# Kernel tuning notes

Measured on AMD Instinct MI355X. Metric: run time of the kernel, lower is better.

## Reference

```python
import jax, jax.numpy as jnp
import numpy as np

B_SZ, SEQ, ENC = 8, 768, 21
PRED = 192
N_HIPPO = 256
MULTISCALE = [1, 2, 4]
MODES = 32  # min(32, min(pred_len, seq_len)//2)


def _transition(N):
    Q = np.arange(N, dtype=np.float64)
    R = (2 * Q + 1)[:, None]
    j, i = np.meshgrid(Q, Q)
    A = np.where(i < j, -1.0, (-1.0) ** (i - j + 1)) * R
    Bv = (-1.0) ** Q[:, None] * R
    return A, Bv


def _hippo_discrete(N, dt):
    # scipy cont2discrete bilinear (Tustin, alpha=0.5)
    A, Bv = _transition(N)
    I = np.eye(N)
    M = I - (dt / 2.0) * A
    Ad = np.linalg.solve(M, I + (dt / 2.0) * A)
    Bd = np.linalg.solve(M, dt * Bv).squeeze(-1)
    return (jnp.asarray(Ad, jnp.float32), jnp.asarray(Bd, jnp.float32))


def _eval_matrix(N, dt):
    # ss.eval_legendre(arange(N)[:,None], 1-2*vals).T  -> (len(vals), N)
    vals = np.arange(0.0, 1.0, dt)
    x = 1.0 - 2.0 * vals
    P = np.zeros((len(vals), N), dtype=np.float64)
    P[:, 0] = 1.0
    if N > 1:
        P[:, 1] = x
    for n in range(1, N - 1):
        P[:, n + 1] = ((2 * n + 1) * x * P[:, n] - n * P[:, n - 1]) / (n + 1)
    return jnp.asarray(P, jnp.float32)


def _legt(x, A, Bv):
    # x: (B, E, L) -> HiPPO coeffs (B, E, N, L) via linear recurrence
    fs = jnp.moveaxis(x, -1, 0)  # (L, B, E)
    c0 = jnp.zeros(x.shape[:-1] + (A.shape[0],), x.dtype)

    def step(c, f):
        c = c @ A.T + f[..., None] * Bv
        return c, c

    _, cs = jax.lax.scan(step, c0, fs)  # (L, B, E, N)
    return jnp.moveaxis(cs, 0, -1)  # (B, E, N, L)


def _spectral(x, wr, wi):
    # x: (B, E, N_in, L); wr/wi: (N_in, N_out, MODES)
    L = x.shape[-1]
    xft = jnp.fft.rfft(x)
    a = xft[..., :MODES]
    o_re = jnp.einsum('bjix,iox->bjox', a.real, wr) - jnp.einsum('bjix,iox->bjox', a.imag, wi)
    o_im = jnp.einsum('bjix,iox->bjox', a.real, wi) + jnp.einsum('bjix,iox->bjox', a.imag, wr)
    o = jax.lax.complex(o_re, o_im)
    pad = jnp.zeros(o.shape[:-1] + (L // 2 + 1 - MODES,), o.dtype)
    return jnp.fft.irfft(jnp.concatenate([o, pad], axis=-1), n=L)


def _forward(x_enc, affine_weight, affine_bias, spec_wr, spec_wi, mlp_w, mlp_b):
    means = jax.lax.stop_gradient(jnp.mean(x_enc, axis=1, keepdims=True))
    xc = x_enc - means
    stdev = jax.lax.stop_gradient(jnp.sqrt(jnp.var(xc, axis=1, keepdims=True) + 1e-5))
    xc = xc / stdev
    xc = xc * affine_weight + affine_bias

    x_decs = []
    for i, m in enumerate(MULTISCALE):
        dt = 1.0 / PRED / m
        A, Bv = _hippo_discrete(N_HIPPO, dt)
        ev = _eval_matrix(N_HIPPO, dt)  # (m*PRED, N)
        x_in = xc[:, -m * PRED:]  # (B, L, E)
        c = _legt(jnp.transpose(x_in, (0, 2, 1)), A, Bv)  # (B, E, N, L)
        out1 = _spectral(c, spec_wr[i], spec_wi[i])  # (B, E, N, L)
        # seq_len >= pred_len branch: take time index PRED-1 along L
        x_dec_c = out1[:, :, :, PRED - 1].swapaxes(-1, -1)  # (B, E, N) after transpose(2,3) + index
        x_dec_c = out1.swapaxes(2, 3)[:, :, PRED - 1, :]  # (B, E, N)
        x_dec = x_dec_c @ ev[-PRED:, :].T  # (B, E, PRED)
        x_decs.append(x_dec)

    xd = jnp.stack(x_decs, axis=-1)  # (B, E, PRED, 3)
    xd = jnp.einsum('beps,os->bepo', xd, mlp_w) + mlp_b  # Linear(3,1)
    xd = jnp.transpose(xd[..., 0], (0, 2, 1))  # (B, PRED, E)
    xd = (xd - affine_bias) / (affine_weight + 1e-10)
    xd = xd * stdev + means
    return xd


def setup_inputs() -> dict:
    key = jax.random.key(0)
    ks = jax.random.split(key, 8)
    scale = 1.0 / (N_HIPPO * N_HIPPO)
    return {
        'x_enc': jax.random.normal(ks[0], (B_SZ, SEQ, ENC), jnp.float32),
        'x_mark_enc': jax.random.normal(ks[1], (B_SZ, SEQ, 4), jnp.float32),
        'x_dec_true': jax.random.normal(ks[2], (B_SZ, 240, ENC), jnp.float32),
        'x_mark_dec': jax.random.normal(ks[3], (B_SZ, 240, 4), jnp.float32),
        'affine_weight': jnp.ones((1, 1, ENC), jnp.float32),
        'affine_bias': jnp.zeros((1, 1, ENC), jnp.float32),
        'spec_wr': scale * jax.random.uniform(ks[4], (3, N_HIPPO, N_HIPPO, MODES), jnp.float32),
        'spec_wi': scale * jax.random.uniform(ks[5], (3, N_HIPPO, N_HIPPO, MODES), jnp.float32),
        'mlp_w': jax.random.normal(ks[6], (1, 3), jnp.float32) * 0.3,
        'mlp_b': jnp.zeros((1,), jnp.float32),
    }


def reference(x_enc, x_mark_enc, x_dec_true, x_mark_dec, affine_weight, affine_bias,
              spec_wr, spec_wi, mlp_w, mlp_b):
    # x_mark_enc / x_dec_true / x_mark_dec are unused by the forecast path (as in torch).
    return _forward(x_enc, affine_weight, affine_bias, spec_wr, spec_wi, mlp_w, mlp_b)
```

## Files before the change

### kernel.cpp

```cpp
#include <hip/hip_runtime.h>
#include <vector>
#include <cmath>
#include <cstring>

#define PI_D 3.14159265358979323846

typedef unsigned short ushort_t;
typedef __attribute__((ext_vector_type(8))) short bf16x8;
typedef __attribute__((ext_vector_type(4))) float f32x4;

#define CF_TRIG_F 0
#define CF_EVP_F  192
#define CF_FLOATS 147648
#define CU_USHORTS 688128
#define CONST_BYTES (CF_FLOATS*4 + CU_USHORTS*2)

#define OFF_XCT   0
#define OFF_MEANS 129024
#define OFF_STD   129280
#define OFF_OUT1  129536
#define OFF_XP1P  258560
#define OFF_PART  1161728
#define OFF_AHI   5290496
#define OFF_ALO   9419264
#define OFF_FB2   13548032
#define OFF_YF    26130944
#define OFF_CFALL 40581632

static const int L_S[3] = {192, 384, 768};


static inline unsigned short h_f2b(float v) {
  unsigned int u; memcpy(&u, &v, 4);
  unsigned int r = (u + 0x7FFF + ((u >> 16) & 1)) >> 16;
  return (unsigned short)r;
}
static inline float h_b2f(unsigned short h) {
  unsigned int u = (unsigned int)h << 16; float f; memcpy(&f, &u, 4); return f;
}

static unsigned char g_consts[CONST_BYTES];

static void compute_consts_host(unsigned char* blob) {
  float* outf = (float*)blob;
  ushort_t* outu = (ushort_t*)(blob + CF_FLOATS * 4);
  const int N = 256;
  for (int s = 0; s < 3; ++s) {
    const int L = L_S[s];
    const int m = 1 << s;
    const double dt = 1.0 / 192.0 / (double)m;

    for (int k = 0; k < 32; ++k) {
      double th = 2.0 * PI_D * (double)k * 191.0 / (double)L;
      outf[CF_TRIG_F + s * 64 + 2 * k]     = (float)cos(th);
      outf[CF_TRIG_F + s * 64 + 2 * k + 1] = (float)sin(th);
    }
    for (int r = 0; r < 192; ++r) {
      int irow = L - 192 + r;
      double x = 1.0 - 2.0 * ((double)irow * dt);
      float* dst = outf + CF_EVP_F + ((size_t)s * 192 + r) * 256;
      double pm1 = 1.0, pc = x;
      dst[0] = 1.0f; dst[1] = (float)x;
      for (int n = 1; n < N - 1; ++n) {
        double pn = ((2.0 * n + 1.0) * x * pc - (double)n * pm1) / (double)(n + 1);
        pm1 = pc; pc = pn;
        dst[n + 1] = (float)pn;
      }
    }
    const int W = N + 257;
    std::vector<double> G((size_t)N * W);
    for (int i = 0; i < N; ++i) {
      double R = 2.0 * i + 1.0;
      for (int j = 0; j < N; ++j) {
        double a = (i < j) ? -R : ((((i - j + 1) & 1) ? -R : R));
        G[(size_t)i * W + j]     = (i == j ? 1.0 : 0.0) - 0.5 * dt * a;
        G[(size_t)i * W + N + j] = (i == j ? 1.0 : 0.0) + 0.5 * dt * a;
      }
      G[(size_t)i * W + N + 256] = dt * (((i & 1) ? -R : R));
    }
    for (int k = 0; k < N; ++k) {
      int piv = k; double best = fabs(G[(size_t)k * W + k]);
      for (int r = k + 1; r < N; ++r) {
        double v = fabs(G[(size_t)r * W + k]);
        if (v > best) { best = v; piv = r; }
      }
      if (piv != k)
        for (int c = k; c < W; ++c) std::swap(G[(size_t)k * W + c], G[(size_t)piv * W + c]);
      double inv = 1.0 / G[(size_t)k * W + k];
      for (int r = k + 1; r < N; ++r) {
        double f = G[(size_t)r * W + k] * inv;
        if (f != 0.0) {
          double* Rr = &G[(size_t)r * W];
          const double* Rk = &G[(size_t)k * W];
          for (int c = k; c < W; ++c) Rr[c] -= f * Rk[c];
        }
      }
    }
    std::vector<double> X((size_t)N * 257);
    for (int k = N - 1; k >= 0; --k) {
      double inv = 1.0 / G[(size_t)k * W + k];
      const double* Rk = &G[(size_t)k * W];
      for (int c = 0; c < 257; ++c) {
        double v = Rk[N + c];
        for (int j = k + 1; j < N; ++j) v -= Rk[j] * X[(size_t)j * 257 + c];
        X[(size_t)k * 257 + c] = v * inv;
      }
    }
    std::vector<double> Ad((size_t)N * N), kvec(N), knew(N);
    for (int i = 0; i < N; ++i)
      for (int j = 0; j < N; ++j)
        Ad[(size_t)i * N + j] = (double)(float)X[(size_t)i * 257 + j];
    for (int i = 0; i < N; ++i) kvec[i] = (double)(float)X[(size_t)i * 257 + 256];

    ushort_t* fkt = outu + 98304 * ((1 << s) - 1);
    for (int d = 0; d < L; ++d) {
      if (d > 0) {
        for (int i = 0; i < N; ++i) {
          const double* row = &Ad[(size_t)i * N];
          double acc = 0.0;
          for (int j = 0; j < N; ++j) acc += row[j] * kvec[j];
          knew[i] = acc;
        }
        kvec.swap(knew);
      }
      for (int n = 0; n < N; ++n) {
        float kv = (float)kvec[n];
        unsigned short hi = h_f2b(kv);
        unsigned short lo = h_f2b(kv - h_b2f(hi));
        size_t base = ((size_t)((d >> 5) * 16 + (n >> 4)) * 2) * 512
                    + (size_t)((d & 31) >> 3) * 128 + (size_t)(n & 15) * 8 + (d & 7);
        fkt[base]       = hi;
        fkt[base + 512] = lo;
      }
    }
  }
}

static bool  g_dev_ok  = false;
static void* g_dev_ptr = nullptr;

namespace {
struct ConstInit {
  ConstInit() {
    compute_consts_host(g_consts);
    void* p = nullptr;
    if (hipMalloc(&p, CONST_BYTES) == hipSuccess && p != nullptr) {
      if (hipMemcpy(p, g_consts, CONST_BYTES, hipMemcpyHostToDevice) == hipSuccess) {
        g_dev_ptr = p;
        g_dev_ok  = true;
      } else {
        (void)hipFree(p);
      }
    }
    (void)hipHostRegister((void*)g_consts, sizeof(g_consts), hipHostRegisterDefault);
  }
};
static ConstInit g_const_init;
}

__device__ inline unsigned short f2b(float v) {
  unsigned int u = __float_as_uint(v);
  unsigned int r = (u + 0x7FFF + ((u >> 16) & 1)) >> 16;
  return (unsigned short)r;
}
__device__ inline float b2f(unsigned short h) {
  return __uint_as_float((unsigned int)h << 16);
}
__device__ inline unsigned int pack2(float a, float b) {
  return (unsigned int)f2b(a) | ((unsigned int)f2b(b) << 16);
}

__device__ inline float blockReduceSum(float v) {
  __shared__ float sm[4];
  #pragma unroll
  for (int off = 32; off > 0; off >>= 1) v += __shfl_down(v, off);
  int wid = threadIdx.x >> 6, lane = threadIdx.x & 63;
  if (lane == 0) sm[wid] = v;
  __syncthreads();
  if (threadIdx.x == 0) sm[0] = sm[0] + sm[1] + sm[2] + sm[3];
  __syncthreads();
  float r = sm[0];
  __syncthreads();
  return r;
}

__global__ __launch_bounds__(256) void norm_kernel(
    const float* __restrict__ x_enc, const float* __restrict__ aw,
    const float* __restrict__ ab, float* __restrict__ xcT,
    float* __restrict__ means, float* __restrict__ stdev) {
  int bj = blockIdx.x; int b = bj / 21, j = bj % 21;
  const float* xp = x_enc + (size_t)b * 768 * 21 + j;
  int tid = threadIdx.x;
  float lv[3]; float s = 0.f;
  #pragma unroll
  for (int i = 0; i < 3; ++i) { lv[i] = xp[(size_t)(tid + 256 * i) * 21]; s += lv[i]; }
  float tot = blockReduceSum(s);
  float mean = tot * (1.0f / 768.0f);
  float v = 0.f;
  #pragma unroll
  for (int i = 0; i < 3; ++i) { float d = lv[i] - mean; v += d * d; }
  float totv = blockReduceSum(v);
  float sd = sqrtf(totv * (1.0f / 768.0f) + 1e-5f);
  if (tid == 0) { means[bj] = mean; stdev[bj] = sd; }
  float wj = aw[j], bjv = ab[j];
  #pragma unroll
  for (int i = 0; i < 3; ++i)
    xcT[(size_t)bj * 768 + tid + 256 * i] = ((lv[i] - mean) / sd) * wj + bjv;
}

__global__ __launch_bounds__(256) void xp1_kernel(
    const float* __restrict__ xcT, double2* __restrict__ P) {
  int tid = blockIdx.x * 256 + threadIdx.x;
  if (tid >= 5376 * 42) return;
  int nk = tid % 5376, cg = tid / 5376;
  int scale = (cg < 6) ? 0 : (cg < 18 ? 1 : 2);
  int c = cg - 6 * ((1 << scale) - 1);
  int L = 192 << scale;
  int bj = nk >> 5, k = nk & 31;
  const float* x = xcT + (size_t)bj * 768 + (768 - L);
  int u0 = c * 32;
  double ang = -2.0 * PI_D * (double)((k * u0) % L) / (double)L;
  double re = cos(ang), im = sin(ang);
  double wang = -2.0 * PI_D * (double)k / (double)L;
  double cw = cos(wang), sw = sin(wang);
  double sre = 0.0, sim = 0.0;
  #pragma unroll 8
  for (int j = 0; j < 32; ++j) {
    double xv = (double)x[u0 + j];
    sre += xv * re; sim += xv * im;
    double nr = re * cw - im * sw, ni = re * sw + im * cw;
    re = nr; im = ni;
  }
  P[(size_t)cg * 5376 + nk] = make_double2(sre, sim);
}

__global__ __launch_bounds__(256) void xp2_kernel(
    const float* __restrict__ xcT, const double2* __restrict__ P,
    ushort_t* __restrict__ YF) {
  int tid = blockIdx.x * 256 + threadIdx.x;
  if (tid >= 5376 * 42) return;
  int nk = tid % 5376, cg = tid / 5376;
  int scale = (cg < 6) ? 0 : (cg < 18 ? 1 : 2);
  int cbase = 6 * ((1 << scale) - 1);
  int c = cg - cbase;
  int L = 192 << scale;
  ushort_t* FA = YF + (size_t)4128768 * ((1 << scale) - 1);
  int bj = nk >> 5, k = nk & 31;
  const float* x = xcT + (size_t)bj * 768 + (768 - L);
  double bre = 0.0, bim = 0.0;
  for (int cc = cbase; cc < cg; ++cc) {
    double2 p = P[(size_t)cc * 5376 + nk];
    bre += p.x; bim += p.y;
  }
  int u0 = c * 32;
  double ang = -2.0 * PI_D * (double)((k * u0) % L) / (double)L;
  double ure = cos(ang), uim = sin(ang);
  double wang = -2.0 * PI_D * (double)k / (double)L;
  double cw = cos(wang), sw = sin(wang);
  int d0 = L - 1 - u0;
  double angd = -2.0 * PI_D * (double)((k * d0) % L) / (double)L;
  double dre = cos(angd), dim = sin(angd);

  float vre_buf[32], vim_buf[32];
  #pragma unroll
  for (int j = 0; j < 32; ++j) {
    double xv = (double)x[u0 + j];
    bre += xv * ure; bim += xv * uim;
    int m = 31 - j;
    vre_buf[m] = (float)(dre * bre - dim * bim);
    vim_buf[m] = (float)(dre * bim + dim * bre);
    double t1 = ure * cw - uim * sw, t2 = ure * sw + uim * cw;
    ure = t1; uim = t2;
    double t3 = dre * cw + dim * sw, t4 = dim * cw - dre * sw;
    dre = t3; dim = t4;
  }

  int nK0 = L >> 5;
  int K0 = (d0 - 31) >> 5;
  int rre = bj * 64 + k * 2;
  int rim = rre + 1;
  size_t baseRe = (((size_t)(rre >> 4) * nK0 + K0) * 2) * 512 + (size_t)(rre & 15) * 8;
  size_t baseIm = (((size_t)(rim >> 4) * nK0 + K0) * 2) * 512 + (size_t)(rim & 15) * 8;
  #pragma unroll
  for (int q = 0; q < 4; ++q) {
    float f0 = vre_buf[q*8+0], f1 = vre_buf[q*8+1], f2 = vre_buf[q*8+2], f3 = vre_buf[q*8+3];
    float f4 = vre_buf[q*8+4], f5 = vre_buf[q*8+5], f6 = vre_buf[q*8+6], f7 = vre_buf[q*8+7];
    uint4 vh = make_uint4(pack2(f0,f1), pack2(f2,f3), pack2(f4,f5), pack2(f6,f7));
    uint4 vl = make_uint4(pack2(f0-b2f(f2b(f0)), f1-b2f(f2b(f1))),
                          pack2(f2-b2f(f2b(f2)), f3-b2f(f2b(f3))),
                          pack2(f4-b2f(f2b(f4)), f5-b2f(f2b(f5))),
                          pack2(f6-b2f(f2b(f6)), f7-b2f(f2b(f7))));
    *(uint4*)(FA + baseRe + q*128)       = vh;
    *(uint4*)(FA + baseRe + 512 + q*128) = vl;
  }
  #pragma unroll
  for (int q = 0; q < 4; ++q) {
    float f0 = vim_buf[q*8+0], f1 = vim_buf[q*8+1], f2 = vim_buf[q*8+2], f3 = vim_buf[q*8+3];
    float f4 = vim_buf[q*8+4], f5 = vim_buf[q*8+5], f6 = vim_buf[q*8+6], f7 = vim_buf[q*8+7];
    uint4 vh = make_uint4(pack2(f0,f1), pack2(f2,f3), pack2(f4,f5), pack2(f6,f7));
    uint4 vl = make_uint4(pack2(f0-b2f(f2b(f0)), f1-b2f(f2b(f1))),
                          pack2(f2-b2f(f2b(f2)), f3-b2f(f2b(f3))),
                          pack2(f4-b2f(f2b(f4)), f5-b2f(f2b(f5))),
                          pack2(f6-b2f(f2b(f6)), f7-b2f(f2b(f7))));
    *(uint4*)(FA + baseIm + q*128)       = vh;
    *(uint4*)(FA + baseIm + 512 + q*128) = vl;
  }
}

__global__ __launch_bounds__(512) void wb_kernel(
    const float* __restrict__ wrS_all, const float* __restrict__ wiS_all,
    const float* __restrict__ trig_all, ushort_t* __restrict__ FB2_all) {
  int s = blockIdx.z;
  const float* wrS = wrS_all + (size_t)s * 256 * 256 * 32;
  const float* wiS = wiS_all + (size_t)s * 256 * 256 * 32;
  const float* trig = trig_all + s * 64;
  ushort_t* FB2 = FB2_all + (size_t)s * 8388608;
  int L = 192 << s;
  int t = threadIdx.x;
  int of = blockIdx.x;
  int nsb = blockIdx.y;
  int lgk = t >> 7;
  int e   = t & 7;
  int om  = (t >> 3) & 15;
  int nstate = nsb * 32 + lgk * 8 + e;
  int o = of * 16 + om;
  const float* wrp = wrS + ((size_t)nstate * 256 + o) * 32;
  const float* wip = wiS + ((size_t)nstate * 256 + o) * 32;
  float invL = 1.0f / (float)L;
  #pragma unroll 4
  for (int k = 0; k < 32; ++k) {
    float ck = trig[2 * k], sk = trig[2 * k + 1];
    float fk = (k == 0 ? 1.0f : 2.0f) * invL;
    float wr = wrp[k], wi = wip[k];
    float vre = fk * (wr * ck - wi * sk);
    float vim = fk * (-wi * ck - wr * sk);
    int qre = (k * 2) * 8 + nsb;
    size_t bre = ((size_t)(qre * 16 + of) * 2) * 512 + t;
    size_t bim = ((size_t)((qre + 8) * 16 + of) * 2) * 512 + t;
    unsigned short hre = f2b(vre), him = f2b(vim);
    FB2[bre]       = hre;
    FB2[bre + 512] = f2b(vre - b2f(hre));
    FB2[bim]       = him;
    FB2[bim + 512] = f2b(vim - b2f(him));
  }
}

__global__ __launch_bounds__(768, 3) void gemm1_mfma(
    const ushort_t* __restrict__ YF, const ushort_t* __restrict__ KTall,
    ushort_t* __restrict__ AHI, ushort_t* __restrict__ ALO) {
  const int s = blockIdx.y;
  const int K = 192 << s;
  const ushort_t* FA = YF + (size_t)4128768 * ((1 << s) - 1);
  const ushort_t* FB = KTall + (size_t)98304 * ((1 << s) - 1);
  ushort_t* Chi = AHI + (size_t)2752512 * s;
  ushort_t* Clo = ALO + (size_t)2752512 * s;

  const int wave = threadIdx.x >> 6;
  const int lane = threadIdx.x & 63;
  const int li = lane & 15, lg = lane >> 4;
  const int mh = wave >> 2;
  const int nw = wave & 3;
  const int bn = nw * 64;
  const int nK0 = K >> 5;
  const int strip = blockIdx.x * 3 + mh;
  const int bm = strip * 16;
  const int nf0 = nw * 4;

  bf16x8 aH0, aL0, bH0[4], bL0[4];
  bf16x8 aH1, aL1, bH1[4], bL1[4];
  bf16x8 aH2, aL2, bH2[4], bL2[4];
  f32x4 acc[4] = {};

  #define G1_LOAD(AH, AL, BH, BL, K0_) {                                      \
    size_t fa = ((size_t)(strip * nK0 + (K0_)) * 2) * 512 + lane * 8;         \
    AH = *(const bf16x8*)(FA + fa);                                           \
    AL = *(const bf16x8*)(FA + fa + 512);                                     \
    _Pragma("unroll")                                                         \
    for (int nf = 0; nf < 4; ++nf) {                                          \
      size_t fb = ((size_t)((K0_) * 16 + nf0 + nf) * 2) * 512 + lane * 8;     \
      BH[nf] = *(const bf16x8*)(FB + fb);                                     \
      BL[nf] = *(const bf16x8*)(FB + fb + 512);                               \
    } }

  #define G1_MFMA(AH, AL, BH, BL) {                                          \
    _Pragma("unroll")                                                        \
    for (int nf = 0; nf < 4; ++nf) {                                         \
      acc[nf] = __builtin_amdgcn_mfma_f32_16x16x32_bf16(AH, BH[nf], acc[nf], 0, 0, 0); \
      acc[nf] = __builtin_amdgcn_mfma_f32_16x16x32_bf16(AH, BL[nf], acc[nf], 0, 0, 0); \
      acc[nf] = __builtin_amdgcn_mfma_f32_16x16x32_bf16(AL, BH[nf], acc[nf], 0, 0, 0); \
    } }

  G1_LOAD(aH0, aL0, bH0, bL0, 0);
  G1_LOAD(aH1, aL1, bH1, bL1, 1);
  G1_LOAD(aH2, aL2, bH2, bL2, 2);
  for (int K0 = 0; K0 < nK0; K0 += 3) {
    G1_MFMA(aH0, aL0, bH0, bL0);
    if (K0 + 3 < nK0) G1_LOAD(aH0, aL0, bH0, bL0, K0 + 3);
    G1_MFMA(aH1, aL1, bH1, bL1);
    if (K0 + 4 < nK0) G1_LOAD(aH1, aL1, bH1, bL1, K0 + 4);
    G1_MFMA(aH2, aL2, bH2, bL2);
    if (K0 + 5 < nK0) G1_LOAD(aH2, aL2, bH2, bL2, K0 + 5);
  }
  #undef G1_LOAD
  #undef G1_MFMA

  #pragma unroll
  for (int r = 0; r < 4; ++r) {
    int row = bm + lg * 4 + r;
    #pragma unroll
    for (int nf = 0; nf < 4; ++nf) {
      int col = bn + nf * 16 + li;
      float v = acc[nf][r];
      unsigned short hi = f2b(v);
      Chi[(size_t)row * 256 + col] = hi;
      Clo[(size_t)row * 256 + col] = f2b(v - b2f(hi));
    }
  }
}

__global__ __launch_bounds__(256) void gemm2_mfma(
    const ushort_t* __restrict__ AHI, const ushort_t* __restrict__ ALO,
    const ushort_t* __restrict__ FB2_all, float* __restrict__ PART) {
  const int zz = blockIdx.z;
  const int s = zz >> 5;
  const int z = zz & 31;
  const ushort_t* Ahi = AHI + (size_t)2752512 * s;
  const ushort_t* Alo = ALO + (size_t)2752512 * s;
  const ushort_t* FB2 = FB2_all + (size_t)s * 8388608;
  float* C = PART + (size_t)s * 1376256 + (size_t)z * 43008;

  const int wave = threadIdx.x >> 6;
  const int lane = threadIdx.x & 63;
  const int li = lane & 15, lg = lane >> 4;
  const int bm = blockIdx.y * 64;
  const int bn = blockIdx.x * 64;
  const int nf0 = blockIdx.x * 4;
  const int ks = z * 512;

  const int rowA = bm + wave * 16 + li;
  const bool aok = (rowA < 168);
  const size_t aoff = (size_t)(aok ? rowA : 0) * 16384;

  bf16x8 aH0, aL0, bH0[4], bL0[4];
  bf16x8 aH1, aL1, bH1[4], bL1[4];
  f32x4 acc[4] = {};

  #define G2_LOAD(AH, AL, BH, BL, KC_) {                                   \
    int kc_ = (KC_) + lg * 8;                                              \
    if (aok) { AH = *(const bf16x8*)(Ahi + aoff + kc_);                    \
               AL = *(const bf16x8*)(Alo + aoff + kc_); }                  \
    else     { AH = (bf16x8)(short)0; AL = (bf16x8)(short)0; }             \
    int q_ = (KC_) >> 5;                                                   \
    _Pragma("unroll")                                                      \
    for (int nf = 0; nf < 4; ++nf) {                                       \
      size_t fb = ((size_t)(q_ * 16 + nf0 + nf) * 2) * 512 + lane * 8;     \
      BH[nf] = *(const bf16x8*)(FB2 + fb);                                 \
      BL[nf] = *(const bf16x8*)(FB2 + fb + 512);                           \
    } }

  #define G2_MFMA(AH, AL, BH, BL) {                                        \
    _Pragma("unroll")                                                      \
    for (int nf = 0; nf < 4; ++nf) {                                       \
      acc[nf] = __builtin_amdgcn_mfma_f32_16x16x32_bf16(AH, BH[nf], acc[nf], 0, 0, 0); \
      acc[nf] = __builtin_amdgcn_mfma_f32_16x16x32_bf16(AH, BL[nf], acc[nf], 0, 0, 0); \
      acc[nf] = __builtin_amdgcn_mfma_f32_16x16x32_bf16(AL, BH[nf], acc[nf], 0, 0, 0); \
    } }

  G2_LOAD(aH0, aL0, bH0, bL0, ks);
  for (int k0 = ks; k0 < ks + 512; k0 += 64) {
    G2_LOAD(aH1, aL1, bH1, bL1, k0 + 32);
    G2_MFMA(aH0, aL0, bH0, bL0);
    if (k0 + 64 < ks + 512) G2_LOAD(aH0, aL0, bH0, bL0, k0 + 64);
    G2_MFMA(aH1, aL1, bH1, bL1);
  }
  #undef G2_LOAD
  #undef G2_MFMA

  #pragma unroll
  for (int r = 0; r < 4; ++r) {
    int row = bm + wave * 16 + lg * 4 + r;
    if (row < 168) {
      #pragma unroll
      for (int nf = 0; nf < 4; ++nf) {
        int col = bn + nf * 16 + li;
        C[(size_t)row * 256 + col] = acc[nf][r];
      }
    }
  }
}

__global__ __launch_bounds__(256) void reduce_kernel(
    const float* __restrict__ PART, float* __restrict__ OUT1) {
  int s = blockIdx.y;
  int e = blockIdx.x * 256 + threadIdx.x;
  const float* part = PART + (size_t)s * 1376256;
  float sum = 0.f;
  for (int c = 0; c < 32; ++c) sum += part[(size_t)c * 43008 + e];
  OUT1[(size_t)s * 43008 + e] = sum;
}

__global__ __launch_bounds__(256) void final_kernel(
    const float* __restrict__ out1, const float* __restrict__ evp,
    const float* __restrict__ means, const float* __restrict__ stdev,
    const float* __restrict__ aw, const float* __restrict__ ab,
    const float* __restrict__ mlp_w, const float* __restrict__ mlp_b,
    float* __restrict__ out) {
  int tid = blockIdx.x * 256 + threadIdx.x;
  int j = tid % 21; int bp = tid / 21; int p = bp % 192; int b = bp / 192;
  int bj = b * 21 + j;
  float acc = mlp_b[0];
  #pragma unroll
  for (int s = 0; s < 3; ++s) {
    const float* o1 = out1 + ((size_t)s * 168 + bj) * 256;
    const float* ev = evp + ((size_t)s * 192 + p) * 256;
    float d = 0.f;
    #pragma unroll 4
    for (int n = 0; n < 256; ++n) d = fmaf(o1[n], ev[n], d);
    acc = fmaf(mlp_w[s], d, acc);
  }
  float v = (acc - ab[j]) / (aw[j] + 1e-10f);
  out[tid] = v * stdev[bj] + means[bj];
}

extern "C" void kernel_launch(void* const* d_in, const int* in_sizes, int n_in,
                              void* d_out, int out_size, void* d_ws, size_t ws_size,
                              hipStream_t stream) {
  const float* x_enc   = (const float*)d_in[0];
  const float* aw      = (const float*)d_in[4];
  const float* ab      = (const float*)d_in[5];
  const float* spec_wr = (const float*)d_in[6];
  const float* spec_wi = (const float*)d_in[7];
  const float* mlp_w   = (const float*)d_in[8];
  const float* mlp_b   = (const float*)d_in[9];
  float* wsf = (float*)d_ws;
  float* out = (float*)d_out;

  const unsigned char* cst_base;
  if (g_dev_ok) {
    cst_base = (const unsigned char*)g_dev_ptr;
  } else {
    hipMemcpyAsync(wsf + OFF_CFALL, g_consts, CONST_BYTES,
                   hipMemcpyHostToDevice, stream);
    cst_base = (const unsigned char*)(wsf + OFF_CFALL);
  }
  const float*    cst_f  = (const float*)cst_base;
  const ushort_t* cst_us = (const ushort_t*)(cst_base + CF_FLOATS * 4);

  ushort_t* yf  = (ushort_t*)(wsf + OFF_YF);
  ushort_t* ahi = (ushort_t*)(wsf + OFF_AHI);
  ushort_t* alo = (ushort_t*)(wsf + OFF_ALO);
  ushort_t* fb2 = (ushort_t*)(wsf + OFF_FB2);

  norm_kernel<<<168, 256, 0, stream>>>(x_enc, aw, ab,
      wsf + OFF_XCT, wsf + OFF_MEANS, wsf + OFF_STD);

  xp1_kernel<<<(5376 * 42 + 255) / 256, 256, 0, stream>>>(
      wsf + OFF_XCT, (double2*)(wsf + OFF_XP1P));
  xp2_kernel<<<(5376 * 42 + 255) / 256, 256, 0, stream>>>(
      wsf + OFF_XCT, (const double2*)(wsf + OFF_XP1P), yf);
  wb_kernel<<<dim3(16, 8, 3), 512, 0, stream>>>(
      spec_wr, spec_wi, cst_f + CF_TRIG_F, fb2);
  gemm1_mfma<<<dim3(224, 3), 768, 0, stream>>>(
      yf, cst_us, ahi, alo);
  gemm2_mfma<<<dim3(4, 3, 96), 256, 0, stream>>>(
      ahi, alo, fb2, wsf + OFF_PART);
  reduce_kernel<<<dim3(168, 3), 256, 0, stream>>>(
      wsf + OFF_PART, wsf + OFF_OUT1);

  final_kernel<<<126, 256, 0, stream>>>(
      wsf + OFF_OUT1, cst_f + CF_EVP_F, wsf + OFF_MEANS, wsf + OFF_STD,
      aw, ab, mlp_w, mlp_b, out);
}
```

Before: 208.5 us.

## Use float twiddle recurrences in DFT prep kernels and shrink gemm1 blocks

The xp1 and xp2 partial-DFT kernels now run their twiddle rotation and products in fp32 and keep only the running sums in double, cutting the slow FP64 work. Separately, gemm1 is relaunched with 256-thread blocks covering one 16-row strip each instead of 768-thread blocks covering three, which gives the scheduler more and smaller blocks. The fp32 twiddle recurrence over 32 steps may drift and lose accuracy compared with the double version.

```diff
diff --git a/kernel.cpp b/kernel.cpp
--- a/kernel.cpp
+++ b/kernel.cpp
@@ -220,15 +220,15 @@
   const float* x = xcT + (size_t)bj * 768 + (768 - L);
   int u0 = c * 32;
   double ang = -2.0 * PI_D * (double)((k * u0) % L) / (double)L;
-  double re = cos(ang), im = sin(ang);
+  float re = (float)cos(ang), im = (float)sin(ang);
   double wang = -2.0 * PI_D * (double)k / (double)L;
-  double cw = cos(wang), sw = sin(wang);
+  float cw = (float)cos(wang), sw = (float)sin(wang);
   double sre = 0.0, sim = 0.0;
   #pragma unroll 8
   for (int j = 0; j < 32; ++j) {
-    double xv = (double)x[u0 + j];
-    sre += xv * re; sim += xv * im;
-    double nr = re * cw - im * sw, ni = re * sw + im * cw;
+    float xv = x[u0 + j];
+    sre += (double)(xv * re); sim += (double)(xv * im);
+    float nr = re * cw - im * sw, ni = re * sw + im * cw;
     re = nr; im = ni;
   }
   P[(size_t)cg * 5376 + nk] = make_double2(sre, sim);
@@ -254,24 +254,25 @@
   }
   int u0 = c * 32;
   double ang = -2.0 * PI_D * (double)((k * u0) % L) / (double)L;
-  double ure = cos(ang), uim = sin(ang);
+  float ure = (float)cos(ang), uim = (float)sin(ang);
   double wang = -2.0 * PI_D * (double)k / (double)L;
-  double cw = cos(wang), sw = sin(wang);
+  float cw = (float)cos(wang), sw = (float)sin(wang);
   int d0 = L - 1 - u0;
   double angd = -2.0 * PI_D * (double)((k * d0) % L) / (double)L;
-  double dre = cos(angd), dim = sin(angd);
+  float dre = (float)cos(angd), dim = (float)sin(angd);
 
   float vre_buf[32], vim_buf[32];
   #pragma unroll
   for (int j = 0; j < 32; ++j) {
-    double xv = (double)x[u0 + j];
-    bre += xv * ure; bim += xv * uim;
+    float xv = x[u0 + j];
+    bre += (double)(xv * ure); bim += (double)(xv * uim);
+    float brf = (float)bre, bif = (float)bim;
     int m = 31 - j;
-    vre_buf[m] = (float)(dre * bre - dim * bim);
-    vim_buf[m] = (float)(dre * bim + dim * bre);
-    double t1 = ure * cw - uim * sw, t2 = ure * sw + uim * cw;
+    vre_buf[m] = dre * brf - dim * bif;
+    vim_buf[m] = dre * bif + dim * brf;
+    float t1 = ure * cw - uim * sw, t2 = ure * sw + uim * cw;
     ure = t1; uim = t2;
-    double t3 = dre * cw + dim * sw, t4 = dim * cw - dre * sw;
+    float t3 = dre * cw + dim * sw, t4 = dim * cw - dre * sw;
     dre = t3; dim = t4;
   }
 
@@ -345,7 +346,7 @@
   }
 }
 
-__global__ __launch_bounds__(768, 3) void gemm1_mfma(
+__global__ __launch_bounds__(256, 6) void gemm1_mfma(
     const ushort_t* __restrict__ YF, const ushort_t* __restrict__ KTall,
     ushort_t* __restrict__ AHI, ushort_t* __restrict__ ALO) {
   const int s = blockIdx.y;
@@ -358,13 +359,11 @@
   const int wave = threadIdx.x >> 6;
   const int lane = threadIdx.x & 63;
   const int li = lane & 15, lg = lane >> 4;
-  const int mh = wave >> 2;
-  const int nw = wave & 3;
-  const int bn = nw * 64;
+  const int bn = wave * 64;
   const int nK0 = K >> 5;
-  const int strip = blockIdx.x * 3 + mh;
+  const int strip = blockIdx.x;
   const int bm = strip * 16;
-  const int nf0 = nw * 4;
+  const int nf0 = wave * 4;
 
   bf16x8 aH0, aL0, bH0[4], bL0[4];
   bf16x8 aH1, aL1, bH1[4], bL1[4];
@@ -560,7 +559,7 @@
       wsf + OFF_XCT, (const double2*)(wsf + OFF_XP1P), yf);
   wb_kernel<<<dim3(16, 8, 3), 512, 0, stream>>>(
       spec_wr, spec_wi, cst_f + CF_TRIG_F, fb2);
-  gemm1_mfma<<<dim3(224, 3), 768, 0, stream>>>(
+  gemm1_mfma<<<dim3(672, 3), 256, 0, stream>>>(
       yf, cst_us, ahi, alo);
   gemm2_mfma<<<dim3(4, 3, 96), 256, 0, stream>>>(
       ahi, alo, fb2, wsf + OFF_PART);
```

After: 486.2 us. 2.33x slower.
